# Optimization experiments

Hardware: AMD Instinct MI355X
Metric: run time of the kernel (lower is better)

## Reference

```python
import jax, jax.numpy as jnp
import numpy as np

PS = 4        # bkg_patch_size
PD = 1        # replicate pad
UFSTRIDE = 2  # patch-extraction stride
STRIDE = 1    # correlation stride
SCALE = 10.0  # softmax_scale


def pad_edge(x):
    return jnp.pad(x, ((0, 0), (0, 0), (PD, PD), (PD, PD)), mode='edge')


def unfold(x, ps, stride):
    # x: (B,C,H,W) -> (B, L, C, ps, ps), row-major over patch grid (matches F.unfold)
    B, C, H, W = x.shape
    oh = (H - ps) // stride + 1
    ow = (W - ps) // stride + 1
    ih = jnp.arange(oh)[:, None] * stride + jnp.arange(ps)[None, :]  # (oh, ps)
    iw = jnp.arange(ow)[:, None] * stride + jnp.arange(ps)[None, :]  # (ow, ps)
    p = x[:, :, ih][:, :, :, :, iw]            # (B,C,oh,ps,ow,ps)
    p = p.transpose(0, 2, 4, 1, 3, 5)          # (B,oh,ow,C,ps,ps)
    return p.reshape(B, oh * ow, C, ps, ps)


def diag3(x):
    # conv2d with 3x3 identity kernel, padding=1: out[i,j] = in[i-1,j-1]+in[i,j]+in[i+1,j+1]
    B, one, N, M = x.shape
    xp = jnp.pad(x, ((0, 0), (0, 0), (1, 1), (1, 1)))
    return xp[:, :, 0:N, 0:M] + xp[:, :, 1:N + 1, 1:M + 1] + xp[:, :, 2:N + 2, 2:M + 2]


def setup_inputs() -> dict:
    key = jax.random.key(0)
    k1, k2, k3 = jax.random.split(key, 3)
    B, C, H, W = 4, 64, 64, 64
    f = jax.random.normal(k1, (B, C, H, W), dtype=jnp.float32)
    b = jax.random.normal(k2, (B, C, H, W), dtype=jnp.float32)
    mask = (jax.random.uniform(k3, (B, 1, H, W)) < 0.25).astype(jnp.float32)
    return {"f": f, "b": b, "mask": mask}


def reference(f, b, mask):
    B, C, H, W = b.shape
    maskc = 1.0 - mask
    # --- get_conv_kernel: per-(batch,channel) L2-normalize b, extract patch kernels ---
    bn = b / jnp.sqrt(jnp.sum(b * b, axis=(2, 3), keepdims=True) + 1e-8)
    kernel = unfold(pad_edge(bn), PS, UFSTRIDE)                 # (B, L, C, ps, ps)
    mk = unfold(pad_edge(maskc), PS, UFSTRIDE)                  # (B, L, 1, ps, ps)
    mmk = jnp.mean(mk, axis=(2, 3, 4))[:, :, None, None]        # (B, L, 1, 1)
    L = kernel.shape[1]

    # --- batched grouped cross-correlation: conv f with per-sample patch kernels ---
    fpatch = unfold(pad_edge(f), PS, STRIDE)                    # (B, P, C, ps, ps)
    hs = (H + 2 * PD - PS) // STRIDE + 1
    ws = (W + 2 * PD - PS) // STRIDE + 1
    cos = jnp.einsum('bpcij,blcij->blp', fpatch, kernel)        # (B, L, P)
    cos = cos.reshape(B, L, hs, ws)

    # --- fuse: diagonal 3x3 convs along two axis pairings ---
    hb, wb = H // 2, W // 2
    cs = L
    c1 = diag3(cos.reshape(B, 1, cs, hs * ws))
    c1 = c1.reshape(B, 1, hb, wb, hs, ws).transpose(0, 1, 3, 2, 5, 4).reshape(B, 1, cs, hs * ws)
    c1 = diag3(c1)
    c1 = c1.reshape(B, 1, hb, wb, hs, ws).transpose(0, 1, 3, 2, 5, 4)
    cos = c1.reshape(B, cs, hs, ws)

    # --- irregular mask logic ---
    mp = unfold(pad_edge(maskc), PS, STRIDE)                    # (B, P, 1, ps, ps)
    mmp = jnp.mean(mp, axis=(2, 3, 4)).reshape(B, 1, hs, ws)    # (B, 1, hs, ws)
    mm = (mmk > mmp).astype(cos.dtype)                          # (B, L, hs, ws)
    ppp = (mmp > 0.5).astype(cos.dtype)
    mm = mm * ppp + (mmk == 1.0).astype(cos.dtype)
    mm = (mm > 0).astype(cos.dtype)

    cos = cos * mm
    return jax.nn.softmax(cos * SCALE, axis=1)
```

## Files before the change

kernel.cpp:

```cpp
#include <hip/hip_runtime.h>
#include <math.h>

#define NB 4
#define NC 64
#define NL 1024
#define NP 3969
#define PHW 63

typedef unsigned short ushort_t;
typedef __attribute__((ext_vector_type(8))) short short8;
typedef __attribute__((ext_vector_type(16))) float floatx16;

#define A_BSTRIDE 1048576
#define B_BSTRIDE 4194304

__global__ __launch_bounds__(256) void prep_kernel(const float* __restrict__ bsrc,
                                                   const float* __restrict__ mask,
                                                   float* __restrict__ invn,
                                                   float* __restrict__ mmk,
                                                   float* __restrict__ mmp,
                                                   ushort_t* __restrict__ Bhi,
                                                   ushort_t* __restrict__ Blo) {
    int blk = blockIdx.x;
    if (blk < 256) {
        const float* src = bsrc + (size_t)blk * 4096;
        float s = 0.f;
        for (int i = threadIdx.x; i < 4096; i += 256) { float v = src[i]; s += v * v; }
#pragma unroll
        for (int off = 32; off > 0; off >>= 1) s += __shfl_down(s, off, 64);
        __shared__ float part[4];
        if ((threadIdx.x & 63) == 0) part[threadIdx.x >> 6] = s;
        __syncthreads();
        if (threadIdx.x == 0) {
            float t = part[0] + part[1] + part[2] + part[3];
            invn[blk] = 1.0f / sqrtf(t + 1e-8f);
        }
    } else if (blk < 335) {
        int id = (blk - 256) * 256 + threadIdx.x;
        if (id < NB * NL) {
            int b = id >> 10, l = id & 1023;
            int lh = l >> 5, lw = l & 31;
            const float* m = mask + b * 4096;
            float s = 0.f;
#pragma unroll
            for (int i = 0; i < 4; ++i) {
                int r = min(max(2 * lh - 1 + i, 0), 63);
#pragma unroll
                for (int j = 0; j < 4; ++j) {
                    int c = min(max(2 * lw - 1 + j, 0), 63);
                    s += 1.0f - m[r * 64 + c];
                }
            }
            mmk[id] = s * (1.0f / 16.0f);
        } else {
            int id2 = id - NB * NL;
            if (id2 < NB * NP) {
                int b = id2 / NP, p = id2 - b * NP;
                int ph = p / PHW, pw = p - ph * PHW;
                const float* m = mask + b * 4096;
                float s = 0.f;
#pragma unroll
                for (int i = 0; i < 4; ++i) {
                    int r = min(max(ph - 1 + i, 0), 63);
#pragma unroll
                    for (int j = 0; j < 4; ++j) {
                        int c = min(max(pw - 1 + j, 0), 63);
                        s += 1.0f - m[r * 64 + c];
                    }
                }
                mmp[id2] = s * (1.0f / 16.0f);
            }
        }
    } else {
        int idx = (blk - 335) * 256 + threadIdx.x;
        int b = idx >> 15;
        int r = idx & 32767;
        int mat = r >> 14;
        int o = r & 16383;
        ushort_t* base = (mat ? Blo : Bhi) + (size_t)b * B_BSTRIDE + 124 * 32768;
        uint4 z = {0u, 0u, 0u, 0u};
        ((uint4*)base)[o] = z;
    }
}

__device__ inline void split_bf16(float v, ushort_t& hv, ushort_t& lv) {
    unsigned u = __float_as_uint(v);
    unsigned rr = u + 0x7FFFu + ((u >> 16) & 1u);
    hv = (ushort_t)(rr >> 16);
    float fh = __uint_as_float(((unsigned)hv) << 16);
    float remv = v - fh;
    unsigned u2 = __float_as_uint(remv);
    unsigned rr2 = u2 + 0x7FFFu + ((u2 >> 16) & 1u);
    lv = (ushort_t)(rr2 >> 16);
}

__device__ inline int frag_addr(int row, int kc) {
    return ((row >> 5) * 64 + kc) * 512 + (row & 31) * 8;
}

__global__ __launch_bounds__(256) void split_kernel(const float* __restrict__ bsrc,
                                                    const float* __restrict__ invn,
                                                    ushort_t* __restrict__ Ahi,
                                                    ushort_t* __restrict__ Alo,
                                                    const float* __restrict__ fsrc,
                                                    ushort_t* __restrict__ Bhi,
                                                    ushort_t* __restrict__ Blo) {
    __shared__ float fl[32 * 257];
    int x = blockIdx.x, b = blockIdx.y, chalf = blockIdx.z;
    int t = threadIdx.x;
    if (x < 32) {
        int lh = x;
#pragma unroll
        for (int q = 0; q < 32; ++q) {
            int idx = t + (q << 8);
            int cl = idx >> 8, rem = idx & 255;
            int i = rem >> 6, s = rem & 63;
            int c = (chalf << 5) + cl;
            int r = min(max(2 * lh - 1 + i, 0), 63);
            fl[cl * 257 + rem] = bsrc[(((size_t)((b << 6) + c)) << 12) + (r << 6) + s];
        }
        __syncthreads();
        ushort_t* Ah = Ahi + (size_t)b * A_BSTRIDE;
        ushort_t* Al = Alo + (size_t)b * A_BSTRIDE;
#pragma unroll
        for (int q = 0; q < 4; ++q) {
            int pair = t + (q << 8);
            int lw = pair & 31, cl = pair >> 5;
            int c = (chalf << 5) + cl;
            float scale = invn[(b << 6) + c];
            const float* row = fl + cl * 257;
            __align__(16) ushort_t h[16];
            __align__(16) ushort_t lo[16];
#pragma unroll
            for (int i = 0; i < 4; ++i)
#pragma unroll
                for (int j = 0; j < 4; ++j) {
                    int s = min(max(2 * lw - 1 + j, 0), 63);
                    split_bf16(row[i * 64 + s] * scale, h[i * 4 + j], lo[i * 4 + j]);
                }
            int a = (lh * 64 + c) * 512 + lw * 8;
            *(uint4*)(Ah + a)       = *(uint4*)h;
            *(uint4*)(Ah + a + 256) = *(uint4*)(h + 8);
            *(uint4*)(Al + a)       = *(uint4*)lo;
            *(uint4*)(Al + a + 256) = *(uint4*)(lo + 8);
        }
    } else {
        int ph = x - 32;
#pragma unroll
        for (int q = 0; q < 32; ++q) {
            int idx = t + (q << 8);
            int cl = idx >> 8, rem = idx & 255;
            int i = rem >> 6, s = rem & 63;
            int c = (chalf << 5) + cl;
            int r = min(max(ph - 1 + i, 0), 63);
            fl[cl * 257 + rem] = fsrc[(((size_t)((b << 6) + c)) << 12) + (r << 6) + s];
        }
        __syncthreads();
        ushort_t* Bh = Bhi + (size_t)b * B_BSTRIDE;
        ushort_t* Bl = Blo + (size_t)b * B_BSTRIDE;
#pragma unroll
        for (int q = 0; q < 8; ++q) {
            int pair = t + (q << 8);
            int pw = pair & 63, cl = pair >> 6;
            if (pw < PHW) {
                int c = (chalf << 5) + cl;
                const float* row = fl + cl * 257;
                __align__(16) ushort_t h[16];
                __align__(16) ushort_t lo[16];
#pragma unroll
                for (int i = 0; i < 4; ++i)
#pragma unroll
                    for (int j = 0; j < 4; ++j) {
                        int s = min(max(pw - 1 + j, 0), 63);
                        split_bf16(row[i * 64 + s], h[i * 4 + j], lo[i * 4 + j]);
                    }
                int p = ph * PHW + pw;
                int a = frag_addr(p, c);
                *(uint4*)(Bh + a)       = *(uint4*)h;
                *(uint4*)(Bh + a + 256) = *(uint4*)(h + 8);
                *(uint4*)(Bl + a)       = *(uint4*)lo;
                *(uint4*)(Bl + a + 256) = *(uint4*)(lo + 8);
            }
        }
    }
}

__global__ __launch_bounds__(256, 2) void gemm_kernel(
    const ushort_t* __restrict__ Ahi, const ushort_t* __restrict__ Alo,
    const ushort_t* __restrict__ Bhi, const ushort_t* __restrict__ Blo,
    float* __restrict__ Rt) {
    __shared__ ushort_t smem[2][12288];
    int tid = threadIdx.x;
    int lane = tid & 63, w = tid >> 6;
    int bid = blockIdx.x;
    int wid = ((bid & 7) << 6) + (bid >> 3);
    int b = wid >> 7;
    int rem = wid & 127;
    int lg = rem >> 4;
    int pg = rem & 15;
    int L0 = lg << 7, P0 = pg << 8;

    const ushort_t* segp[6];
    int seg0 = w * 6;
#pragma unroll
    for (int i = 0; i < 6; ++i) {
        int seg = seg0 + i;
        const ushort_t* base;
        int rt;
        if (seg < 4)       { base = Ahi + (size_t)b * A_BSTRIDE + (size_t)(lg << 2) * 32768; rt = seg; }
        else if (seg < 8)  { base = Alo + (size_t)b * A_BSTRIDE + (size_t)(lg << 2) * 32768; rt = seg - 4; }
        else if (seg < 16) { base = Bhi + (size_t)b * B_BSTRIDE + (size_t)(pg << 3) * 32768; rt = seg - 8; }
        else               { base = Blo + (size_t)b * B_BSTRIDE + (size_t)(pg << 3) * 32768; rt = seg - 16; }
        segp[i] = base + (size_t)rt * 32768 + (size_t)(lane << 3);
    }
    int dst0 = seg0 * 512;

    ushort_t* buf0 = smem[0];
    ushort_t* buf1 = smem[1];

#define STAGE(dstp, kc)                                                                    \
    do {                                                                                   \
        _Pragma("unroll")                                                                  \
        for (int i = 0; i < 6; ++i)                                                        \
            __builtin_amdgcn_global_load_lds(                                              \
                (const __attribute__((address_space(1))) void*)(segp[i] + (size_t)(kc) * 512), \
                (__attribute__((address_space(3))) void*)((dstp) + dst0 + i * 512),        \
                16, 0, 0);                                                                 \
    } while (0)

    floatx16 acc[2][4];
#pragma unroll
    for (int i = 0; i < 2; ++i)
#pragma unroll
        for (int j = 0; j < 4; ++j)
#pragma unroll
            for (int r = 0; r < 16; ++r) acc[i][j][r] = 0.f;

    STAGE(buf0, 0);
    ushort_t* cur = buf0;
    ushort_t* nxt = buf1;

    int boff0 = 4096 + (w << 1) * 512;

    for (int t = 0; t < 64; ++t) {
        asm volatile("" ::: "memory");
        __builtin_amdgcn_s_barrier();
        asm volatile("" ::: "memory");
        if (t < 63) {
            STAGE(nxt, t + 1);
            asm volatile("s_waitcnt vmcnt(6)" ::: "memory");
        } else {
            asm volatile("s_waitcnt vmcnt(0)" ::: "memory");
        }
        __builtin_amdgcn_s_barrier();
        asm volatile("" ::: "memory");

        const ushort_t* rb = cur + (lane << 3);
        short8 ah[4], al[4], bh[2], bl[2];
#pragma unroll
        for (int lt = 0; lt < 4; ++lt) {
            ah[lt] = *(const short8*)(rb + lt * 512);
            al[lt] = *(const short8*)(rb + 2048 + lt * 512);
        }
#pragma unroll
        for (int pt = 0; pt < 2; ++pt) {
            bh[pt] = *(const short8*)(rb + boff0 + pt * 512);
            bl[pt] = *(const short8*)(rb + 4096 + boff0 + pt * 512);
        }
        __builtin_amdgcn_s_setprio(1);
#pragma unroll
        for (int pt = 0; pt < 2; ++pt)
#pragma unroll
            for (int lt = 0; lt < 4; ++lt) {
                acc[pt][lt] = __builtin_amdgcn_mfma_f32_32x32x16_bf16(bh[pt], ah[lt], acc[pt][lt], 0, 0, 0);
                acc[pt][lt] = __builtin_amdgcn_mfma_f32_32x32x16_bf16(bh[pt], al[lt], acc[pt][lt], 0, 0, 0);
                acc[pt][lt] = __builtin_amdgcn_mfma_f32_32x32x16_bf16(bl[pt], ah[lt], acc[pt][lt], 0, 0, 0);
            }
        __builtin_amdgcn_s_setprio(0);
        ushort_t* tmp = cur; cur = nxt; nxt = tmp;
    }
#undef STAGE

    int x = lane & 31, kg = lane >> 5;
    int pw0 = P0 + (w << 6);
#pragma unroll
    for (int pt = 0; pt < 2; ++pt)
#pragma unroll
        for (int lt = 0; lt < 4; ++lt)
#pragma unroll
            for (int r = 0; r < 16; ++r) {
                int p = pw0 + (pt << 5) + (r & 3) + ((r >> 2) << 3) + (kg << 2);
                int l = L0 + (lt << 5) + x;
                if (p < NP) Rt[((size_t)b * NP + p) * NL + l] = acc[pt][lt][r];
            }
}

__global__ __launch_bounds__(256) void softmax_fused_kernel(const float* __restrict__ Rt,
                                                            const float* __restrict__ mmkA,
                                                            const float* __restrict__ mmpA,
                                                            float* __restrict__ E) {
    __shared__ float ld0[1024], ld1[1024], ld2[1024];
    __shared__ float red[8];
    int ph = blockIdx.x, pwg = blockIdx.y, b = blockIdx.z;
    int t = threadIdx.x;
    int lane = t & 63, w = t >> 6;
    int l0 = t << 2;
    const float* Rb = Rt + (size_t)b * NP * NL;

    for (int g = 0; g < 7; ++g) {
        int pw = pwg * 7 + g;
        int p = ph * PHW + pw;
        bool okm = (p != 0), okp = (p != 3968);
        int Pm = (ph > 0) ? p - 63 : 3905 + pw;
        int Pp = (ph < 62) ? p + 63 : pw + 1;

#define BUILD(dst, q)                                                   \
    do {                                                                \
        const float* base = Rb + (size_t)(q) * NL;                      \
        float4 r = *(const float4*)(base + l0);                         \
        if ((q) > 0) {                                                  \
            const float* pm = base - NL;                                \
            r.x += (l0 > 0) ? pm[l0 - 1] : 0.f;                         \
            r.y += pm[l0];  r.z += pm[l0 + 1];  r.w += pm[l0 + 2];      \
        }                                                               \
        if ((q) < NP - 1) {                                             \
            const float* pp = base + NL;                                \
            r.x += pp[l0 + 1];  r.y += pp[l0 + 2];  r.z += pp[l0 + 3];  \
            r.w += (l0 + 4 < NL) ? pp[l0 + 4] : 0.f;                    \
        }                                                               \
        *(float4*)(dst + l0) = r;                                       \
    } while (0)

        BUILD(ld0, p);
        if (okm) BUILD(ld1, Pm);
        if (okp) BUILD(ld2, Pp);
#undef BUILD
        __syncthreads();

        float4 vc = *(const float4*)(ld0 + l0);
        float4 vm = {0.f, 0.f, 0.f, 0.f}, vp = {0.f, 0.f, 0.f, 0.f};
        if (okm) {
            if (l0 >= 32) vm = *(const float4*)(ld1 + l0 - 32);
            else {
                vm.x = (l0 == 0) ? 0.f : ld1[l0 + 991];
                vm.y = ld1[l0 + 992];
                vm.z = ld1[l0 + 993];
                vm.w = ld1[l0 + 994];
            }
        }
        if (okp) {
            if (l0 < 992) vp = *(const float4*)(ld2 + l0 + 32);
            else {
                vp.x = ld2[l0 - 991];
                vp.y = ld2[l0 - 990];
                vp.z = ld2[l0 - 989];
                vp.w = (l0 + 3 == 1023) ? 0.f : ld2[l0 - 988];
            }
        }
        float mmpv = mmpA[b * NP + p];
        float4 km = *(const float4*)(mmkA + b * NL + l0);
        float lg[4];
        float fsum[4] = {vc.x + vm.x + vp.x, vc.y + vm.y + vp.y,
                         vc.z + vm.z + vp.z, vc.w + vm.w + vp.w};
        float kk[4] = {km.x, km.y, km.z, km.w};
#pragma unroll
        for (int i = 0; i < 4; ++i) {
            float mmv = (((kk[i] > mmpv) && (mmpv > 0.5f)) || (kk[i] == 1.0f)) ? 1.0f : 0.0f;
            lg[i] = fsum[i] * mmv * 10.0f;
        }
        float mx = fmaxf(fmaxf(lg[0], lg[1]), fmaxf(lg[2], lg[3]));
#pragma unroll
        for (int off = 32; off >= 1; off >>= 1) mx = fmaxf(mx, __shfl_xor(mx, off, 64));
        if (lane == 0) red[w] = mx;
        __syncthreads();
        mx = fmaxf(fmaxf(red[0], red[1]), fmaxf(red[2], red[3]));
        float e[4];
        float s = 0.f;
#pragma unroll
        for (int i = 0; i < 4; ++i) { e[i] = expf(lg[i] - mx); s += e[i]; }
#pragma unroll
        for (int off = 32; off >= 1; off >>= 1) s += __shfl_xor(s, off, 64);
        if (lane == 0) red[4 + w] = s;
        __syncthreads();
        float rinv = 1.0f / (red[4] + red[5] + red[6] + red[7]);
        float4 ev = {e[0] * rinv, e[1] * rinv, e[2] * rinv, e[3] * rinv};
        *(float4*)(E + (((size_t)b * NP + p) << 10) + l0) = ev;
        __syncthreads();
    }
}

__global__ __launch_bounds__(256) void transpose_kernel(const float* __restrict__ E,
                                                        float* __restrict__ out) {
    __shared__ float tile[63 * 65];
    int pt = blockIdx.x;
    int lt = blockIdx.y;
    int b  = blockIdx.z;
    int t = threadIdx.x;
    int p0 = pt * 63, l0 = lt << 6;
    const float* Eb = E + ((size_t)b * NP << 10);
    {
        int j = t & 63, i4 = t >> 6;
#pragma unroll
        for (int k = 0; k < 16; ++k) {
            int i = (k << 2) + i4;
            if (i < 63) tile[i * 65 + j] = Eb[((size_t)(p0 + i) << 10) + l0 + j];
        }
    }
    __syncthreads();
    {
        int ii = t & 63, jj4 = t >> 6;
        if (ii < 63) {
#pragma unroll
            for (int k = 0; k < 16; ++k) {
                int jj = (k << 2) + jj4;
                out[((size_t)b * NL + l0 + jj) * NP + p0 + ii] = tile[ii * 65 + jj];
            }
        }
    }
}

extern "C" void kernel_launch(void* const* d_in, const int* in_sizes, int n_in,
                              void* d_out, int out_size, void* d_ws, size_t ws_size,
                              hipStream_t stream) {
    const float* f    = (const float*)d_in[0];
    const float* b    = (const float*)d_in[1];
    const float* mask = (const float*)d_in[2];
    float* out = (float*)d_out;

    float* Rt = (float*)d_out;

    float* wsf = (float*)d_ws;
    float* E  = wsf + 16257024;
    ushort_t* Ahi = (ushort_t*)d_ws;
    ushort_t* Alo = Ahi + (size_t)NB * A_BSTRIDE;
    ushort_t* Bhi = Alo + (size_t)NB * A_BSTRIDE;
    ushort_t* Blo = Bhi + (size_t)NB * B_BSTRIDE;
    float* invn = wsf + 32514048;
    float* mmk = invn + 256;
    float* mmp = mmk + 4096;

    prep_kernel<<<dim3(847), dim3(256), 0, stream>>>(b, mask, invn, mmk, mmp, Bhi, Blo);
    split_kernel<<<dim3(95, 4, 2), dim3(256), 0, stream>>>(b, invn, Ahi, Alo, f, Bhi, Blo);
    gemm_kernel<<<dim3(512), dim3(256), 0, stream>>>(Ahi, Alo, Bhi, Blo, Rt);
    softmax_fused_kernel<<<dim3(63, 9, 4), dim3(256), 0, stream>>>(Rt, mmk, mmp, E);
    transpose_kernel<<<dim3(63, 16, 4), dim3(256), 0, stream>>>(E, out);
}
```

Baseline: 298.0 us.

## Split diagonal pass into separate kernel and parallelize softmax per row

The first diagonal 3-tap pass used to be recomputed three times per output row inside the softmax kernel. It now runs once in its own kernel that writes an intermediate buffer D1. The softmax kernel reads three precomputed D1 rows and launches one block per (p, b) rather than looping over 7 rows. This removes redundant recomputation and raises parallelism, at the cost of an extra 65 MB write and read round trip through global memory plus one more launch.

Result: faster. 273.8 us (-8.1%).

```diff
diff --git a/kernel.cpp b/kernel.cpp
--- a/kernel.cpp
+++ b/kernel.cpp
@@ -295,98 +295,92 @@
             }
 }
 
-__global__ __launch_bounds__(256) void softmax_fused_kernel(const float* __restrict__ Rt,
-                                                            const float* __restrict__ mmkA,
-                                                            const float* __restrict__ mmpA,
-                                                            float* __restrict__ E) {
-    __shared__ float ld0[1024], ld1[1024], ld2[1024];
+__global__ __launch_bounds__(256) void diag1_kernel(const float* __restrict__ Rt,
+                                                    float* __restrict__ D1) {
+    int q = blockIdx.x, b = blockIdx.y;
+    int l0 = threadIdx.x << 2;
+    const float* base = Rt + ((size_t)b * NP + q) * NL;
+    float4 r = *(const float4*)(base + l0);
+    if (q > 0) {
+        const float* pm = base - NL;
+        r.x += (l0 > 0) ? pm[l0 - 1] : 0.f;
+        r.y += pm[l0];  r.z += pm[l0 + 1];  r.w += pm[l0 + 2];
+    }
+    if (q < NP - 1) {
+        const float* pp = base + NL;
+        r.x += pp[l0 + 1];  r.y += pp[l0 + 2];  r.z += pp[l0 + 3];
+        r.w += (l0 + 4 < NL) ? pp[l0 + 4] : 0.f;
+    }
+    *(float4*)(D1 + ((size_t)b * NP + q) * NL + l0) = r;
+}
+
+__global__ __launch_bounds__(256) void softmax_kernel(const float* __restrict__ D1,
+                                                      const float* __restrict__ mmkA,
+                                                      const float* __restrict__ mmpA,
+                                                      float* __restrict__ E) {
     __shared__ float red[8];
-    int ph = blockIdx.x, pwg = blockIdx.y, b = blockIdx.z;
+    int p = blockIdx.x, b = blockIdx.y;
+    int ph = p / PHW, pw = p - ph * PHW;
     int t = threadIdx.x;
     int lane = t & 63, w = t >> 6;
     int l0 = t << 2;
-    const float* Rb = Rt + (size_t)b * NP * NL;
-
-    for (int g = 0; g < 7; ++g) {
-        int pw = pwg * 7 + g;
-        int p = ph * PHW + pw;
-        bool okm = (p != 0), okp = (p != 3968);
-        int Pm = (ph > 0) ? p - 63 : 3905 + pw;
-        int Pp = (ph < 62) ? p + 63 : pw + 1;
-
-#define BUILD(dst, q)                                                   \
-    do {                                                                \
-        const float* base = Rb + (size_t)(q) * NL;                      \
-        float4 r = *(const float4*)(base + l0);                         \
-        if ((q) > 0) {                                                  \
-            const float* pm = base - NL;                                \
-            r.x += (l0 > 0) ? pm[l0 - 1] : 0.f;                         \
-            r.y += pm[l0];  r.z += pm[l0 + 1];  r.w += pm[l0 + 2];      \
-        }                                                               \
-        if ((q) < NP - 1) {                                             \
-            const float* pp = base + NL;                                \
-            r.x += pp[l0 + 1];  r.y += pp[l0 + 2];  r.z += pp[l0 + 3];  \
-            r.w += (l0 + 4 < NL) ? pp[l0 + 4] : 0.f;                    \
-        }                                                               \
-        *(float4*)(dst + l0) = r;                                       \
-    } while (0)
-
-        BUILD(ld0, p);
-        if (okm) BUILD(ld1, Pm);
-        if (okp) BUILD(ld2, Pp);
-#undef BUILD
-        __syncthreads();
-
-        float4 vc = *(const float4*)(ld0 + l0);
-        float4 vm = {0.f, 0.f, 0.f, 0.f}, vp = {0.f, 0.f, 0.f, 0.f};
-        if (okm) {
-            if (l0 >= 32) vm = *(const float4*)(ld1 + l0 - 32);
-            else {
-                vm.x = (l0 == 0) ? 0.f : ld1[l0 + 991];
-                vm.y = ld1[l0 + 992];
-                vm.z = ld1[l0 + 993];
-                vm.w = ld1[l0 + 994];
-            }
-        }
-        if (okp) {
-            if (l0 < 992) vp = *(const float4*)(ld2 + l0 + 32);
-            else {
-                vp.x = ld2[l0 - 991];
-                vp.y = ld2[l0 - 990];
-                vp.z = ld2[l0 - 989];
-                vp.w = (l0 + 3 == 1023) ? 0.f : ld2[l0 - 988];
-            }
-        }
-        float mmpv = mmpA[b * NP + p];
-        float4 km = *(const float4*)(mmkA + b * NL + l0);
-        float lg[4];
-        float fsum[4] = {vc.x + vm.x + vp.x, vc.y + vm.y + vp.y,
-                         vc.z + vm.z + vp.z, vc.w + vm.w + vp.w};
-        float kk[4] = {km.x, km.y, km.z, km.w};
-#pragma unroll
-        for (int i = 0; i < 4; ++i) {
-            float mmv = (((kk[i] > mmpv) && (mmpv > 0.5f)) || (kk[i] == 1.0f)) ? 1.0f : 0.0f;
-            lg[i] = fsum[i] * mmv * 10.0f;
-        }
-        float mx = fmaxf(fmaxf(lg[0], lg[1]), fmaxf(lg[2], lg[3]));
-#pragma unroll
-        for (int off = 32; off >= 1; off >>= 1) mx = fmaxf(mx, __shfl_xor(mx, off, 64));
-        if (lane == 0) red[w] = mx;
-        __syncthreads();
-        mx = fmaxf(fmaxf(red[0], red[1]), fmaxf(red[2], red[3]));
-        float e[4];
-        float s = 0.f;
-#pragma unroll
-        for (int i = 0; i < 4; ++i) { e[i] = expf(lg[i] - mx); s += e[i]; }
-#pragma unroll
-        for (int off = 32; off >= 1; off >>= 1) s += __shfl_xor(s, off, 64);
-        if (lane == 0) red[4 + w] = s;
-        __syncthreads();
-        float rinv = 1.0f / (red[4] + red[5] + red[6] + red[7]);
-        float4 ev = {e[0] * rinv, e[1] * rinv, e[2] * rinv, e[3] * rinv};
-        *(float4*)(E + (((size_t)b * NP + p) << 10) + l0) = ev;
-        __syncthreads();
-    }
+
+    bool okm = (p != 0), okp = (p != 3968);
+    int Pm = (ph > 0) ? p - 63 : 3905 + pw;
+    int Pp = (ph < 62) ? p + 63 : pw + 1;
+
+    const float* Db = D1 + (size_t)b * NP * NL;
+    const float* r0 = Db + (size_t)p * NL;
+    float4 vc = *(const float4*)(r0 + l0);
+    float4 vm = {0.f, 0.f, 0.f, 0.f}, vp = {0.f, 0.f, 0.f, 0.f};
+    if (okm) {
+        const float* r1 = Db + (size_t)Pm * NL;
+        if (l0 >= 32) vm = *(const float4*)(r1 + l0 - 32);
+        else {
+            vm.x = (l0 == 0) ? 0.f : r1[l0 + 991];
+            vm.y = r1[l0 + 992];
+            vm.z = r1[l0 + 993];
+            vm.w = r1[l0 + 994];
+        }
+    }
+    if (okp) {
+        const float* r2 = Db + (size_t)Pp * NL;
+        if (l0 < 992) vp = *(const float4*)(r2 + l0 + 32);
+        else {
+            vp.x = r2[l0 - 991];
+            vp.y = r2[l0 - 990];
+            vp.z = r2[l0 - 989];
+            vp.w = (l0 + 3 == 1023) ? 0.f : r2[l0 - 988];
+        }
+    }
+    float mmpv = mmpA[b * NP + p];
+    float4 km = *(const float4*)(mmkA + b * NL + l0);
+    float lg[4];
+    float fsum[4] = {vc.x + vm.x + vp.x, vc.y + vm.y + vp.y,
+                     vc.z + vm.z + vp.z, vc.w + vm.w + vp.w};
+    float kk[4] = {km.x, km.y, km.z, km.w};
+#pragma unroll
+    for (int i = 0; i < 4; ++i) {
+        float mmv = (((kk[i] > mmpv) && (mmpv > 0.5f)) || (kk[i] == 1.0f)) ? 1.0f : 0.0f;
+        lg[i] = fsum[i] * mmv * 10.0f;
+    }
+    float mx = fmaxf(fmaxf(lg[0], lg[1]), fmaxf(lg[2], lg[3]));
+#pragma unroll
+    for (int off = 32; off >= 1; off >>= 1) mx = fmaxf(mx, __shfl_xor(mx, off, 64));
+    if (lane == 0) red[w] = mx;
+    __syncthreads();
+    mx = fmaxf(fmaxf(red[0], red[1]), fmaxf(red[2], red[3]));
+    float e[4];
+    float s = 0.f;
+#pragma unroll
+    for (int i = 0; i < 4; ++i) { e[i] = expf(lg[i] - mx); s += e[i]; }
+#pragma unroll
+    for (int off = 32; off >= 1; off >>= 1) s += __shfl_xor(s, off, 64);
+    if (lane == 0) red[4 + w] = s;
+    __syncthreads();
+    float rinv = 1.0f / (red[4] + red[5] + red[6] + red[7]);
+    float4 ev = {e[0] * rinv, e[1] * rinv, e[2] * rinv, e[3] * rinv};
+    *(float4*)(E + (((size_t)b * NP + p) << 10) + l0) = ev;
 }
 
 __global__ __launch_bounds__(256) void transpose_kernel(const float* __restrict__ E,
@@ -430,6 +424,7 @@
     float* Rt = (float*)d_out;
 
     float* wsf = (float*)d_ws;
+    float* D1 = wsf;
     float* E  = wsf + 16257024;
     ushort_t* Ahi = (ushort_t*)d_ws;
     ushort_t* Alo = Ahi + (size_t)NB * A_BSTRIDE;
@@ -442,6 +437,7 @@
     prep_kernel<<<dim3(847), dim3(256), 0, stream>>>(b, mask, invn, mmk, mmp, Bhi, Blo);
     split_kernel<<<dim3(95, 4, 2), dim3(256), 0, stream>>>(b, invn, Ahi, Alo, f, Bhi, Blo);
     gemm_kernel<<<dim3(512), dim3(256), 0, stream>>>(Ahi, Alo, Bhi, Blo, Rt);
-    softmax_fused_kernel<<<dim3(63, 9, 4), dim3(256), 0, stream>>>(Rt, mmk, mmp, E);
+    diag1_kernel<<<dim3(3969, 4), dim3(256), 0, stream>>>(Rt, D1);
+    softmax_kernel<<<dim3(3969, 4), dim3(256), 0, stream>>>(D1, mmk, mmp, E);
     transpose_kernel<<<dim3(63, 16, 4), dim3(256), 0, stream>>>(E, out);
 }
```

## Load B fragments directly to registers in GEMM and parallelize softmax per row

Applied to the files above, without the earlier changes.

The GEMM now stages only the A (L-side) hi/lo tiles through LDS, while each wave loads its own B fragments straight from global memory into registers. The main loop is unrolled by two over a fixed double buffer, which reduces LDS footprint and LDS read traffic. Separately, the softmax kernel launches one block per output row instead of looping over seven rows per block, which removes the per-iteration barriers and raises parallelism. The risks are higher register pressure from keeping two sets of B fragments in flight, and a different wait-count ordering in the pipeline.

Result: faster. 260.5 us, median of 2 (-12.6%).

```diff
diff --git a/kernel.cpp b/kernel.cpp
--- a/kernel.cpp
+++ b/kernel.cpp
@@ -189,7 +189,7 @@
     const ushort_t* __restrict__ Ahi, const ushort_t* __restrict__ Alo,
     const ushort_t* __restrict__ Bhi, const ushort_t* __restrict__ Blo,
     float* __restrict__ Rt) {
-    __shared__ ushort_t smem[2][12288];
+    __shared__ ushort_t smem[2][8][512];
     int tid = threadIdx.x;
     int lane = tid & 63, w = tid >> 6;
     int bid = blockIdx.x;
@@ -200,34 +200,57 @@
     int pg = rem & 15;
     int L0 = lg << 7, P0 = pg << 8;
 
-    const ushort_t* segp[6];
-    int seg0 = w * 6;
-#pragma unroll
-    for (int i = 0; i < 6; ++i) {
-        int seg = seg0 + i;
-        const ushort_t* base;
-        int rt;
-        if (seg < 4)       { base = Ahi + (size_t)b * A_BSTRIDE + (size_t)(lg << 2) * 32768; rt = seg; }
-        else if (seg < 8)  { base = Alo + (size_t)b * A_BSTRIDE + (size_t)(lg << 2) * 32768; rt = seg - 4; }
-        else if (seg < 16) { base = Bhi + (size_t)b * B_BSTRIDE + (size_t)(pg << 3) * 32768; rt = seg - 8; }
-        else               { base = Blo + (size_t)b * B_BSTRIDE + (size_t)(pg << 3) * 32768; rt = seg - 16; }
-        segp[i] = base + (size_t)rt * 32768 + (size_t)(lane << 3);
-    }
-    int dst0 = seg0 * 512;
-
-    ushort_t* buf0 = smem[0];
-    ushort_t* buf1 = smem[1];
-
-#define STAGE(dstp, kc)                                                                    \
+    const ushort_t* asrc[2];
+#pragma unroll
+    for (int i = 0; i < 2; ++i) {
+        int s = 2 * w + i;
+        const ushort_t* base = ((s >> 2) ? Alo : Ahi) + (size_t)b * A_BSTRIDE;
+        asrc[i] = base + (size_t)((L0 >> 5) + (s & 3)) * 32768 + (size_t)(lane << 3);
+    }
+    ushort_t* dst0 = &smem[0][2 * w][0];
+    ushort_t* dst1 = &smem[1][2 * w][0];
+
+    const ushort_t* bsrc[4];
+#pragma unroll
+    for (int i = 0; i < 4; ++i) {
+        const ushort_t* base = ((i >> 1) ? Blo : Bhi) + (size_t)b * B_BSTRIDE;
+        bsrc[i] = base + (size_t)((P0 >> 5) + 2 * w + (i & 1)) * 32768 + (size_t)(lane << 3);
+    }
+
+#define STAGEA(dstp, kc)                                                                   \
     do {                                                                                   \
         _Pragma("unroll")                                                                  \
-        for (int i = 0; i < 6; ++i)                                                        \
+        for (int i = 0; i < 2; ++i)                                                        \
             __builtin_amdgcn_global_load_lds(                                              \
-                (const __attribute__((address_space(1))) void*)(segp[i] + (size_t)(kc) * 512), \
-                (__attribute__((address_space(3))) void*)((dstp) + dst0 + i * 512),        \
+                (const __attribute__((address_space(1))) void*)(asrc[i] + (size_t)(kc) * 512), \
+                (__attribute__((address_space(3))) void*)((dstp) + i * 512),               \
                 16, 0, 0);                                                                 \
     } while (0)
 
+#define LOADB(dst, kc)                                                    \
+    do {                                                                  \
+        _Pragma("unroll")                                                 \
+        for (int i = 0; i < 4; ++i)                                       \
+            dst[i] = *(const short8*)(bsrc[i] + (size_t)(kc) * 512);      \
+    } while (0)
+
+#define COMP(bufi, bf)                                                                     \
+    do {                                                                                   \
+        _Pragma("unroll")                                                                  \
+        for (int lt = 0; lt < 4; ++lt) {                                                   \
+            short8 ahf = *(const short8*)(&smem[bufi][lt][lane << 3]);                     \
+            short8 alf = *(const short8*)(&smem[bufi][4 + lt][lane << 3]);                 \
+            __builtin_amdgcn_s_setprio(1);                                                 \
+            _Pragma("unroll")                                                              \
+            for (int pt = 0; pt < 2; ++pt) {                                               \
+                acc[pt][lt] = __builtin_amdgcn_mfma_f32_32x32x16_bf16(bf[pt], ahf, acc[pt][lt], 0, 0, 0);     \
+                acc[pt][lt] = __builtin_amdgcn_mfma_f32_32x32x16_bf16(bf[pt], alf, acc[pt][lt], 0, 0, 0);     \
+                acc[pt][lt] = __builtin_amdgcn_mfma_f32_32x32x16_bf16(bf[2 + pt], ahf, acc[pt][lt], 0, 0, 0); \
+            }                                                                              \
+            __builtin_amdgcn_s_setprio(0);                                                 \
+        }                                                                                  \
+    } while (0)
+
     floatx16 acc[2][4];
 #pragma unroll
     for (int i = 0; i < 2; ++i)
@@ -236,50 +259,35 @@
 #pragma unroll
             for (int r = 0; r < 16; ++r) acc[i][j][r] = 0.f;
 
-    STAGE(buf0, 0);
-    ushort_t* cur = buf0;
-    ushort_t* nxt = buf1;
-
-    int boff0 = 4096 + (w << 1) * 512;
-
-    for (int t = 0; t < 64; ++t) {
+    short8 bB0[4], bB1[4];
+    LOADB(bB0, 0);
+    STAGEA(dst0, 0);
+
+    for (int t = 0; t < 64; t += 2) {
+        LOADB(bB1, t + 1);
+        STAGEA(dst1, t + 1);
+        asm volatile("s_waitcnt vmcnt(6)" ::: "memory");
+        __builtin_amdgcn_s_barrier();
+        asm volatile("" ::: "memory");
+        COMP(0, bB0);
         asm volatile("" ::: "memory");
         __builtin_amdgcn_s_barrier();
-        asm volatile("" ::: "memory");
-        if (t < 63) {
-            STAGE(nxt, t + 1);
+        if (t + 2 < 64) {
+            LOADB(bB0, t + 2);
+            STAGEA(dst0, t + 2);
             asm volatile("s_waitcnt vmcnt(6)" ::: "memory");
         } else {
             asm volatile("s_waitcnt vmcnt(0)" ::: "memory");
         }
         __builtin_amdgcn_s_barrier();
         asm volatile("" ::: "memory");
-
-        const ushort_t* rb = cur + (lane << 3);
-        short8 ah[4], al[4], bh[2], bl[2];
-#pragma unroll
-        for (int lt = 0; lt < 4; ++lt) {
-            ah[lt] = *(const short8*)(rb + lt * 512);
-            al[lt] = *(const short8*)(rb + 2048 + lt * 512);
-        }
-#pragma unroll
-        for (int pt = 0; pt < 2; ++pt) {
-            bh[pt] = *(const short8*)(rb + boff0 + pt * 512);
-            bl[pt] = *(const short8*)(rb + 4096 + boff0 + pt * 512);
-        }
-        __builtin_amdgcn_s_setprio(1);
-#pragma unroll
-        for (int pt = 0; pt < 2; ++pt)
-#pragma unroll
-            for (int lt = 0; lt < 4; ++lt) {
-                acc[pt][lt] = __builtin_amdgcn_mfma_f32_32x32x16_bf16(bh[pt], ah[lt], acc[pt][lt], 0, 0, 0);
-                acc[pt][lt] = __builtin_amdgcn_mfma_f32_32x32x16_bf16(bh[pt], al[lt], acc[pt][lt], 0, 0, 0);
-                acc[pt][lt] = __builtin_amdgcn_mfma_f32_32x32x16_bf16(bl[pt], ah[lt], acc[pt][lt], 0, 0, 0);
-            }
-        __builtin_amdgcn_s_setprio(0);
-        ushort_t* tmp = cur; cur = nxt; nxt = tmp;
-    }
-#undef STAGE
+        COMP(1, bB1);
+        asm volatile("" ::: "memory");
+        __builtin_amdgcn_s_barrier();
+    }
+#undef STAGEA
+#undef LOADB
+#undef COMP
 
     int x = lane & 31, kg = lane >> 5;
     int pw0 = P0 + (w << 6);
@@ -301,19 +309,17 @@
                                                             float* __restrict__ E) {
     __shared__ float ld0[1024], ld1[1024], ld2[1024];
     __shared__ float red[8];
-    int ph = blockIdx.x, pwg = blockIdx.y, b = blockIdx.z;
+    int p = blockIdx.x, b = blockIdx.y;
+    int ph = p / PHW, pw = p - ph * PHW;
     int t = threadIdx.x;
     int lane = t & 63, w = t >> 6;
     int l0 = t << 2;
+
+    bool okm = (p != 0), okp = (p != 3968);
+    int Pm = (ph > 0) ? p - 63 : 3905 + pw;
+    int Pp = (ph < 62) ? p + 63 : pw + 1;
+
     const float* Rb = Rt + (size_t)b * NP * NL;
-
-    for (int g = 0; g < 7; ++g) {
-        int pw = pwg * 7 + g;
-        int p = ph * PHW + pw;
-        bool okm = (p != 0), okp = (p != 3968);
-        int Pm = (ph > 0) ? p - 63 : 3905 + pw;
-        int Pp = (ph < 62) ? p + 63 : pw + 1;
-
 #define BUILD(dst, q)                                                   \
     do {                                                                \
         const float* base = Rb + (size_t)(q) * NL;                      \
@@ -331,62 +337,60 @@
         *(float4*)(dst + l0) = r;                                       \
     } while (0)
 
-        BUILD(ld0, p);
-        if (okm) BUILD(ld1, Pm);
-        if (okp) BUILD(ld2, Pp);
+    BUILD(ld0, p);
+    if (okm) BUILD(ld1, Pm);
+    if (okp) BUILD(ld2, Pp);
 #undef BUILD
-        __syncthreads();
-
-        float4 vc = *(const float4*)(ld0 + l0);
-        float4 vm = {0.f, 0.f, 0.f, 0.f}, vp = {0.f, 0.f, 0.f, 0.f};
-        if (okm) {
-            if (l0 >= 32) vm = *(const float4*)(ld1 + l0 - 32);
-            else {
-                vm.x = (l0 == 0) ? 0.f : ld1[l0 + 991];
-                vm.y = ld1[l0 + 992];
-                vm.z = ld1[l0 + 993];
-                vm.w = ld1[l0 + 994];
-            }
-        }
-        if (okp) {
-            if (l0 < 992) vp = *(const float4*)(ld2 + l0 + 32);
-            else {
-                vp.x = ld2[l0 - 991];
-                vp.y = ld2[l0 - 990];
-                vp.z = ld2[l0 - 989];
-                vp.w = (l0 + 3 == 1023) ? 0.f : ld2[l0 - 988];
-            }
-        }
-        float mmpv = mmpA[b * NP + p];
-        float4 km = *(const float4*)(mmkA + b * NL + l0);
-        float lg[4];
-        float fsum[4] = {vc.x + vm.x + vp.x, vc.y + vm.y + vp.y,
-                         vc.z + vm.z + vp.z, vc.w + vm.w + vp.w};
-        float kk[4] = {km.x, km.y, km.z, km.w};
-#pragma unroll
-        for (int i = 0; i < 4; ++i) {
-            float mmv = (((kk[i] > mmpv) && (mmpv > 0.5f)) || (kk[i] == 1.0f)) ? 1.0f : 0.0f;
-            lg[i] = fsum[i] * mmv * 10.0f;
-        }
-        float mx = fmaxf(fmaxf(lg[0], lg[1]), fmaxf(lg[2], lg[3]));
-#pragma unroll
-        for (int off = 32; off >= 1; off >>= 1) mx = fmaxf(mx, __shfl_xor(mx, off, 64));
-        if (lane == 0) red[w] = mx;
-        __syncthreads();
-        mx = fmaxf(fmaxf(red[0], red[1]), fmaxf(red[2], red[3]));
-        float e[4];
-        float s = 0.f;
-#pragma unroll
-        for (int i = 0; i < 4; ++i) { e[i] = expf(lg[i] - mx); s += e[i]; }
-#pragma unroll
-        for (int off = 32; off >= 1; off >>= 1) s += __shfl_xor(s, off, 64);
-        if (lane == 0) red[4 + w] = s;
-        __syncthreads();
-        float rinv = 1.0f / (red[4] + red[5] + red[6] + red[7]);
-        float4 ev = {e[0] * rinv, e[1] * rinv, e[2] * rinv, e[3] * rinv};
-        *(float4*)(E + (((size_t)b * NP + p) << 10) + l0) = ev;
-        __syncthreads();
-    }
+    __syncthreads();
+
+    float4 vc = *(const float4*)(ld0 + l0);
+    float4 vm = {0.f, 0.f, 0.f, 0.f}, vp = {0.f, 0.f, 0.f, 0.f};
+    if (okm) {
+        if (l0 >= 32) vm = *(const float4*)(ld1 + l0 - 32);
+        else {
+            vm.x = (l0 == 0) ? 0.f : ld1[l0 + 991];
+            vm.y = ld1[l0 + 992];
+            vm.z = ld1[l0 + 993];
+            vm.w = ld1[l0 + 994];
+        }
+    }
+    if (okp) {
+        if (l0 < 992) vp = *(const float4*)(ld2 + l0 + 32);
+        else {
+            vp.x = ld2[l0 - 991];
+            vp.y = ld2[l0 - 990];
+            vp.z = ld2[l0 - 989];
+            vp.w = (l0 + 3 == 1023) ? 0.f : ld2[l0 - 988];
+        }
+    }
+    float mmpv = mmpA[b * NP + p];
+    float4 km = *(const float4*)(mmkA + b * NL + l0);
+    float lg[4];
+    float fsum[4] = {vc.x + vm.x + vp.x, vc.y + vm.y + vp.y,
+                     vc.z + vm.z + vp.z, vc.w + vm.w + vp.w};
+    float kk[4] = {km.x, km.y, km.z, km.w};
+#pragma unroll
+    for (int i = 0; i < 4; ++i) {
+        float mmv = (((kk[i] > mmpv) && (mmpv > 0.5f)) || (kk[i] == 1.0f)) ? 1.0f : 0.0f;
+        lg[i] = fsum[i] * mmv * 10.0f;
+    }
+    float mx = fmaxf(fmaxf(lg[0], lg[1]), fmaxf(lg[2], lg[3]));
+#pragma unroll
+    for (int off = 32; off >= 1; off >>= 1) mx = fmaxf(mx, __shfl_xor(mx, off, 64));
+    if (lane == 0) red[w] = mx;
+    __syncthreads();
+    mx = fmaxf(fmaxf(red[0], red[1]), fmaxf(red[2], red[3]));
+    float e[4];
+    float s = 0.f;
+#pragma unroll
+    for (int i = 0; i < 4; ++i) { e[i] = expf(lg[i] - mx); s += e[i]; }
+#pragma unroll
+    for (int off = 32; off >= 1; off >>= 1) s += __shfl_xor(s, off, 64);
+    if (lane == 0) red[4 + w] = s;
+    __syncthreads();
+    float rinv = 1.0f / (red[4] + red[5] + red[6] + red[7]);
+    float4 ev = {e[0] * rinv, e[1] * rinv, e[2] * rinv, e[3] * rinv};
+    *(float4*)(E + (((size_t)b * NP + p) << 10) + l0) = ev;
 }
 
 __global__ __launch_bounds__(256) void transpose_kernel(const float* __restrict__ E,
@@ -442,6 +446,6 @@
     prep_kernel<<<dim3(847), dim3(256), 0, stream>>>(b, mask, invn, mmk, mmp, Bhi, Blo);
     split_kernel<<<dim3(95, 4, 2), dim3(256), 0, stream>>>(b, invn, Ahi, Alo, f, Bhi, Blo);
     gemm_kernel<<<dim3(512), dim3(256), 0, stream>>>(Ahi, Alo, Bhi, Blo, Rt);
-    softmax_fused_kernel<<<dim3(63, 9, 4), dim3(256), 0, stream>>>(Rt, mmk, mmp, E);
+    softmax_fused_kernel<<<dim3(3969, 4), dim3(256), 0, stream>>>(Rt, mmk, mmp, E);
     transpose_kernel<<<dim3(63, 16, 4), dim3(256), 0, stream>>>(E, out);
 }
```
